# Kernel optimization log

Measured on AMD Instinct MI355X. Metric: run time of the kernel, lower is better.

The kernel has to match this reference:

```python
import jax, jax.numpy as jnp
import numpy as np
from jax import lax

_CLIP_MIN = 1e-06
_CLIP_MAX = 1.0
_POS_ALPHA = 0.0005
NUM_CLASSES = 21
RADIUS = 3
HALF_D = RADIUS * RADIUS
POOL = 3
PAD = POOL // 2
IGNORE = 255
LAM = 0.5  # loss_weight_lambda, lambda_way=1


def _max_pool(x):
    # NCHW max pool, kernel=stride=3, padding=1
    return lax.reduce_window(x, -jnp.inf, lax.max,
                             (1, 1, POOL, POOL), (1, 1, POOL, POOL),
                             ((0, 0), (0, 0), (PAD, PAD), (PAD, PAD)))


def _get_pairs(x):
    # stack radius*radius shifted crops -> [N, C, r^2, nh, nw]
    h, w = x.shape[2], x.shape[3]
    nh, nw = h - RADIUS + 1, w - RADIUS + 1
    crops = [x[:, :, y:y + nh, xo:xo + nw] for y in range(RADIUS) for xo in range(RADIUS)]
    return jnp.stack(crops, axis=2)


def _log_det_by_cholesky(m):
    chol = jnp.linalg.cholesky(m)
    return 2.0 * jnp.sum(jnp.log(jnp.diagonal(chol, axis1=-2, axis2=-1) + 1e-08), axis=-1)


def _rmi_lower_bound(labels_4d, probs_4d):
    la = _max_pool(labels_4d)
    pr = _max_pool(probs_4d)
    n, c = la.shape[0], la.shape[1]
    la_v = _get_pairs(la).reshape(n, c, HALF_D, -1)   # [N,C,d,L]
    pr_v = _get_pairs(pr).reshape(n, c, HALF_D, -1)
    la_v = la_v - jnp.mean(la_v, axis=3, keepdims=True)
    pr_v = pr_v - jnp.mean(pr_v, axis=3, keepdims=True)
    la_cov = jnp.einsum('ncdl,ncel->ncde', la_v, la_v)
    pr_cov = jnp.einsum('ncdl,ncel->ncde', pr_v, pr_v)
    eye = jnp.eye(HALF_D, dtype=la_cov.dtype)
    pr_cov_inv = jnp.linalg.inv(pr_cov + eye * _POS_ALPHA)
    la_pr_cov = jnp.einsum('ncdl,ncel->ncde', la_v, pr_v)
    appro_var = la_cov - jnp.einsum('ncde,ncef,ncgf->ncdg', la_pr_cov, pr_cov_inv, la_pr_cov)
    rmi_now = 0.5 * _log_det_by_cholesky(appro_var + eye * _POS_ALPHA)  # [N,C]
    rmi_per_class = jnp.mean(rmi_now.reshape(-1, NUM_CLASSES), axis=0) / float(HALF_D)
    return jnp.sum(rmi_per_class)


def setup_inputs() -> dict:
    key = jax.random.key(0)
    k1, k2 = jax.random.split(key)
    score = jax.random.normal(k1, (4, NUM_CLASSES, 512, 512), dtype=jnp.float32)
    target = jax.random.randint(k2, (4, 512, 512), 0, NUM_CLASSES, dtype=jnp.int64)
    return {"score": score, "target": target}


def reference(score, target):
    # cross entropy with ignore_index=255, mean reduction
    logp = jax.nn.log_softmax(score, axis=1)                      # [N,C,H,W]
    valid_ce = (target != IGNORE)
    safe_t = jnp.where(valid_ce, target, 0)
    nll = -jnp.take_along_axis(logp, safe_t[:, None].astype(jnp.int32), axis=1)[:, 0]
    normal_loss = jnp.sum(jnp.where(valid_ce, nll, 0.0)) / jnp.sum(valid_ce.astype(jnp.float32))

    # valid one-hot labels and masked sigmoid probs
    mask = (target < NUM_CLASSES)                                 # [N,H,W]
    maskf = mask.astype(jnp.float32)
    onehot = jax.nn.one_hot((target * mask).astype(jnp.int32), NUM_CLASSES, dtype=jnp.float32)
    onehot = onehot * maskf[..., None]                            # [N,H,W,C]
    onehot = jnp.transpose(onehot, (0, 3, 1, 2))                  # [N,C,H,W]
    probs = jnp.clip(jax.nn.sigmoid(score) * maskf[:, None], _CLIP_MIN, _CLIP_MAX)

    rmi_loss = _rmi_lower_bound(onehot, probs)
    return LAM * normal_loss + rmi_loss * (1.0 - LAM)
```

## Files before the change

kernel.cpp:

```cpp
#include <hip/hip_runtime.h>
#include <cfloat>
#include <cmath>

#define DEVINL __device__ __forceinline__

constexpr int N_ = 4, C_ = 21, H_ = 512, W_ = 512;
constexpr int P_ = 171;
constexpr int Q_ = 169;
constexpr int NC_ = N_ * C_;
constexpr int HW_ = H_ * W_;
constexpr int PP_ = 29241;
constexpr int PROW_ = 192;
constexpr int PPAD_ = PROW_ * P_;
constexpr int NCOV_ = 189;
constexpr float EPS_ = 5e-4f;
constexpr int RC_ = 43;
constexpr int G_ = 43;
constexpr int HMROW_ = 172;
constexpr int HMPL_ = 512 * HMROW_;

constexpr int NB_CE = 1024;
constexpr int NB_PL = (NC_ * P_ * G_ + 255) / 256;

typedef float f4_t __attribute__((ext_vector_type(4)));
typedef __attribute__((address_space(1))) const void gas_void;
typedef __attribute__((address_space(3))) void las_void;

DEVINL constexpr int tstart(int d) { return d * 9 - d * (d - 1) / 2; }

template <int CTRL>
DEVINL float dpp_add(float v) {
    int x = __builtin_amdgcn_update_dpp(0, __float_as_int(v), CTRL, 0xF, 0xF, false);
    return v + __int_as_float(x);
}

DEVINL float wave_sum63(float v) {
    v = dpp_add<0x111>(v);
    v = dpp_add<0x112>(v);
    v = dpp_add<0x114>(v);
    v = dpp_add<0x118>(v);
    v = dpp_add<0x142>(v);
    v = dpp_add<0x143>(v);
    return v;
}

__global__ __launch_bounds__(256) void k_bits(const int* __restrict__ target,
                                              unsigned* __restrict__ pack,
                                              float* __restrict__ cov) {
    int t = threadIdx.x;
    if (blockIdx.x == 0) {
        for (int k = t; k < NC_ * NCOV_ + 2; k += 256) cov[k] = 0.f;
    }
    int tid = blockIdx.x * 256 + t;
    if (tid >= N_ * PP_) return;
    int cell = tid % PP_;
    int n = tid / PP_;
    int j = cell % P_;
    int i = cell / P_;
    int hl = 3 * i - 1; if (hl < 0) hl = 0;
    int wl = 3 * j - 1; if (wl < 0) wl = 0;
    int hmax = 3 * i + 1, wmax = 3 * j + 1;
    const int* tb = target + (size_t)n * HW_;
    unsigned oh = 0, px = 0;
#pragma unroll
    for (int r = 0; r < 3; ++r) {
        int hh = hl + r;
        bool hv = hh <= hmax;
        const int* trow = tb + hh * W_;
#pragma unroll
        for (int dc = 0; dc < 3; ++dc) {
            int ww = wl + dc;
            int tv = trow[ww];
            if (hv && (ww <= wmax) && tv >= 0 && tv < C_) {
                oh |= 1u << tv;
                px |= 1u << (r * 3 + dc);
            }
        }
    }
    pack[tid] = oh | (px << 23);
}

__global__ __launch_bounds__(256) void k_ce2(const float* __restrict__ score,
                                             const int* __restrict__ target,
                                             float* __restrict__ hm,
                                             float* __restrict__ cov) {
    __shared__ float lds[4 * 1024];
    __shared__ unsigned char lval[1024];
    __shared__ float rn[4], rc[4];
    int b = blockIdx.x;
    int t = threadIdx.x;
    int wv = t >> 6, lane = t & 63;
    int n = b >> 8;
    int brow = (b & 255) * 2;
    int bhw = brow * W_;
    const float* sp0 = score + (size_t)n * C_ * HW_ + bhw;

    int4 t4 = *(const int4*)(target + (size_t)n * HW_ + bhw + t * 4);
    unsigned vb = (unsigned)(t4.x >= 0 && t4.x < C_)
                | ((unsigned)(t4.y >= 0 && t4.y < C_) << 8)
                | ((unsigned)(t4.z >= 0 && t4.z < C_) << 16)
                | ((unsigned)(t4.w >= 0 && t4.w < C_) << 24);
    *(unsigned*)&lval[t * 4] = vb;

    float4 se = {0.f, 0.f, 0.f, 0.f};
    float4 stgt = {0.f, 0.f, 0.f, 0.f};
    float* hmn = hm + (size_t)n * C_ * HMPL_ + (size_t)brow * HMROW_;

    for (int ph = 0; ph < 6; ++ph) {
        int c0 = ph * 4;
        int np = (c0 + 4 <= C_) ? 4 : (C_ - c0);
        if (wv < np) {
            int c = c0 + wv;
#pragma unroll
            for (int k = 0; k < 4; ++k) {
                const float* g = sp0 + (size_t)c * HW_ + k * 256 + lane * 4;
                float* l = &lds[wv * 1024 + k * 256];
                __builtin_amdgcn_global_load_lds((gas_void*)g, (las_void*)l,
                                                 16, 0, 0);
            }
        }
        asm volatile("s_waitcnt vmcnt(0)" ::: "memory");
        __syncthreads();

        for (int u = 0; u < np; ++u) {
            int cc = c0 + u;
            f4_t v = *(const f4_t*)&lds[u * 1024 + t * 4];
            se.x += __expf(v.x);
            se.y += __expf(v.y);
            se.z += __expf(v.z);
            se.w += __expf(v.w);
            if (t4.x == cc) stgt.x = v.x;
            if (t4.y == cc) stgt.y = v.y;
            if (t4.z == cc) stgt.z = v.z;
            if (t4.w == cc) stgt.w = v.w;
        }

        int nit = np * 342;
        for (int it = t; it < nit; it += 256) {
            int u = it / 342;
            int rem = it - u * 342;
            int r = rem / 171;
            int j = rem - r * 171;
            int wl = 3 * j - 1; if (wl < 0) wl = 0;
            int wmax = 3 * j + 1;
            const float* ls = &lds[u * 1024 + r * 512];
            const unsigned char* lv = &lval[r * 512];
            float m = -FLT_MAX;
#pragma unroll
            for (int dc = 0; dc < 3; ++dc) {
                int ww = wl + dc;
                if (ww <= wmax && lv[ww]) m = fmaxf(m, ls[ww]);
            }
            hmn[(size_t)(c0 + u) * HMPL_ + (size_t)r * HMROW_ + j] = m;
        }
        __syncthreads();
    }

    float nll = 0.f, cnt = 0.f;
    if (t4.x != 255) { nll += __logf(se.x) - stgt.x; cnt += 1.f; }
    if (t4.y != 255) { nll += __logf(se.y) - stgt.y; cnt += 1.f; }
    if (t4.z != 255) { nll += __logf(se.z) - stgt.z; cnt += 1.f; }
    if (t4.w != 255) { nll += __logf(se.w) - stgt.w; cnt += 1.f; }

    nll = wave_sum63(nll);
    cnt = wave_sum63(cnt);
    if (lane == 63) { rn[wv] = nll; rc[wv] = cnt; }
    __syncthreads();
    if (t == 0)
        atomicAdd(&cov[NC_ * NCOV_ + 0], rn[0] + rn[1] + rn[2] + rn[3]);
    if (t == 64)
        atomicAdd(&cov[NC_ * NCOV_ + 1], rc[0] + rc[1] + rc[2] + rc[3]);
}

__global__ __launch_bounds__(256) void k_pool2(const float* __restrict__ hm,
                                               const unsigned* __restrict__ pack,
                                               float* __restrict__ pr,
                                               float* __restrict__ la) {
    int tid = blockIdx.x * 256 + threadIdx.x;
    if (tid >= NC_ * P_ * G_) return;
    int g = tid % G_;
    int rest = tid / G_;
    int i = rest % P_;
    int ncidx = rest / P_;
    int n = ncidx / C_;
    int c = ncidx - n * C_;

    int hl = 3 * i - 1; if (hl < 0) hl = 0;
    int nr = (i == 0) ? 2 : 3;
    const float* hp = hm + (size_t)ncidx * HMPL_ + (size_t)hl * HMROW_ + 4 * g;
    f4_t m = {-FLT_MAX, -FLT_MAX, -FLT_MAX, -FLT_MAX};
    for (int rr = 0; rr < nr; ++rr) {
        f4_t v = *(const f4_t*)(hp + (size_t)rr * HMROW_);
        m.x = fmaxf(m.x, v.x);
        m.y = fmaxf(m.y, v.y);
        m.z = fmaxf(m.z, v.z);
        m.w = fmaxf(m.w, v.w);
    }
    const unsigned* pkp = pack + n * PP_ + i * P_ + 4 * g;
    size_t ob = (size_t)ncidx * PPAD_ + (size_t)i * PROW_ + 4 * g;

    float p0 = fminf(fmaxf(__builtin_amdgcn_rcpf(1.f + __expf(-m.x)), 1e-6f), 1.f);
    float p1 = fminf(fmaxf(__builtin_amdgcn_rcpf(1.f + __expf(-m.y)), 1e-6f), 1.f);
    float p2 = fminf(fmaxf(__builtin_amdgcn_rcpf(1.f + __expf(-m.z)), 1e-6f), 1.f);
    pr[ob + 0] = p0; la[ob + 0] = ((pkp[0] >> c) & 1u) ? 1.f : 0.f;
    pr[ob + 1] = p1; la[ob + 1] = ((pkp[1] >> c) & 1u) ? 1.f : 0.f;
    pr[ob + 2] = p2; la[ob + 2] = ((pkp[2] >> c) & 1u) ? 1.f : 0.f;
    if (4 * g + 3 < P_) {
        float p3 = fminf(fmaxf(__builtin_amdgcn_rcpf(1.f + __expf(-m.w)), 1e-6f), 1.f);
        pr[ob + 3] = p3; la[ob + 3] = ((pkp[3] >> c) & 1u) ? 1.f : 0.f;
    }
}

template <int D0, int D1>
DEVINL void cov_tri(const float* __restrict__ X, float* __restrict__ cov,
                    int nc, int r0, int rend, int s2base,
                    int tid, float (*red)[27]) {
    constexpr int NS2 = ((9 - D0) * (10 - D0) - (9 - D1) * (10 - D1)) / 2;
    constexpr int RLO = D0 / 3;
    constexpr int KOFF = tstart(D0);
    float s2[NS2];
#pragma unroll
    for (int k = 0; k < NS2; ++k) s2[k] = 0.f;

    int nitems = (rend - r0) * G_;
    for (int idx = tid; idx < nitems; idx += 256) {
        int lr = idx / G_;
        int q = idx - lr * G_;
        int x0 = q * 4;
        const float* base = X + (size_t)(r0 + lr) * PROW_ + x0;
        float v[3][8];
#pragma unroll
        for (int r = RLO; r < 3; ++r) {
            float4 u0 = *(const float4*)(base + r * PROW_);
            float4 u1 = *(const float4*)(base + r * PROW_ + 4);
            v[r][0] = u0.x; v[r][1] = u0.y; v[r][2] = u0.z; v[r][3] = u0.w;
            v[r][4] = u1.x; v[r][5] = u1.y; v[r][6] = u1.z; v[r][7] = u1.w;
        }
#pragma unroll
        for (int p = 0; p < 4; ++p) {
            if (x0 + p < Q_) {
                int k = 0;
#pragma unroll
                for (int d = D0; d < D1; ++d)
#pragma unroll
                    for (int e = d; e < 9; ++e) {
                        s2[k] += v[d / 3][p + d % 3] * v[e / 3][p + e % 3];
                        ++k;
                    }
            }
        }
    }

    int lane = tid & 63, wv = tid >> 6;
#pragma unroll
    for (int k = 0; k < NS2; ++k) {
        float v2 = wave_sum63(s2[k]);
        if (lane == 63) red[wv][k] = v2;
    }
    __syncthreads();
    if (tid < NS2) {
        float v2 = red[0][tid] + red[1][tid] + red[2][tid] + red[3][tid];
        atomicAdd(&cov[nc * NCOV_ + s2base + KOFF + tid], v2);
    }
}

template <int RA>
DEVINL void cov_ab(const float* __restrict__ A, const float* __restrict__ B,
                   float* __restrict__ cov, int nc, int r0, int rend,
                   int tid, float (*red)[27]) {
    float sab[27];
#pragma unroll
    for (int k = 0; k < 27; ++k) sab[k] = 0.f;

    int nitems = (rend - r0) * G_;
    for (int idx = tid; idx < nitems; idx += 256) {
        int lr = idx / G_;
        int q = idx - lr * G_;
        int x0 = q * 4;
        size_t off = (size_t)(r0 + lr) * PROW_ + x0;
        float a[8];
        {
            float4 u0 = *(const float4*)(A + off + RA * PROW_);
            float4 u1 = *(const float4*)(A + off + RA * PROW_ + 4);
            a[0] = u0.x; a[1] = u0.y; a[2] = u0.z; a[3] = u0.w;
            a[4] = u1.x; a[5] = u1.y; a[6] = u1.z; a[7] = u1.w;
        }
#pragma unroll
        for (int r = 0; r < 3; ++r) {
            float b[8];
            {
                float4 w0 = *(const float4*)(B + off + r * PROW_);
                float4 w1 = *(const float4*)(B + off + r * PROW_ + 4);
                b[0] = w0.x; b[1] = w0.y; b[2] = w0.z; b[3] = w0.w;
                b[4] = w1.x; b[5] = w1.y; b[6] = w1.z; b[7] = w1.w;
            }
#pragma unroll
            for (int p = 0; p < 4; ++p) {
                if (x0 + p < Q_) {
#pragma unroll
                    for (int dm = 0; dm < 3; ++dm)
#pragma unroll
                        for (int e2 = 0; e2 < 3; ++e2)
                            sab[dm * 9 + r * 3 + e2] += a[p + dm] * b[p + e2];
                }
            }
        }
    }

    int lane = tid & 63, wv = tid >> 6;
#pragma unroll
    for (int k = 0; k < 27; ++k) {
        float v2 = wave_sum63(sab[k]);
        if (lane == 63) red[wv][k] = v2;
    }
    __syncthreads();
    if (tid < 27) {
        float v2 = red[0][tid] + red[1][tid] + red[2][tid] + red[3][tid];
        atomicAdd(&cov[nc * NCOV_ + 108 + RA * 27 + tid], v2);
    }
}

DEVINL void cov_s1(const float* __restrict__ LA, const float* __restrict__ PR,
                   float* __restrict__ cov, int nc, int r0, int rend,
                   int tid, float (*red)[27]) {
    float s1a[9], s1b[9];
#pragma unroll
    for (int k = 0; k < 9; ++k) { s1a[k] = 0.f; s1b[k] = 0.f; }

    int nitems = (rend - r0) * G_;
    for (int idx = tid; idx < nitems; idx += 256) {
        int lr = idx / G_;
        int q = idx - lr * G_;
        int x0 = q * 4;
        size_t off = (size_t)(r0 + lr) * PROW_ + x0;
#pragma unroll
        for (int r = 0; r < 3; ++r) {
            float va[8], vb[8];
            {
                float4 u0 = *(const float4*)(LA + off + r * PROW_);
                float4 u1 = *(const float4*)(LA + off + r * PROW_ + 4);
                va[0] = u0.x; va[1] = u0.y; va[2] = u0.z; va[3] = u0.w;
                va[4] = u1.x; va[5] = u1.y; va[6] = u1.z; va[7] = u1.w;
                float4 w0 = *(const float4*)(PR + off + r * PROW_);
                float4 w1 = *(const float4*)(PR + off + r * PROW_ + 4);
                vb[0] = w0.x; vb[1] = w0.y; vb[2] = w0.z; vb[3] = w0.w;
                vb[4] = w1.x; vb[5] = w1.y; vb[6] = w1.z; vb[7] = w1.w;
            }
#pragma unroll
            for (int p = 0; p < 4; ++p) {
                if (x0 + p < Q_) {
#pragma unroll
                    for (int dc = 0; dc < 3; ++dc) {
                        s1a[r * 3 + dc] += va[p + dc];
                        s1b[r * 3 + dc] += vb[p + dc];
                    }
                }
            }
        }
    }

    int lane = tid & 63, wv = tid >> 6;
#pragma unroll
    for (int k = 0; k < 9; ++k) {
        float v2 = wave_sum63(s1a[k]);
        if (lane == 63) red[wv][k] = v2;
    }
#pragma unroll
    for (int k = 0; k < 9; ++k) {
        float v2 = wave_sum63(s1b[k]);
        if (lane == 63) red[wv][9 + k] = v2;
    }
    __syncthreads();
    if (tid < 18) {
        float v2 = red[0][tid] + red[1][tid] + red[2][tid] + red[3][tid];
        atomicAdd(&cov[nc * NCOV_ + tid], v2);
    }
}

__global__ __launch_bounds__(256) void k_cov(const float* __restrict__ la,
                                             const float* __restrict__ pr,
                                             float* __restrict__ cov) {
    __shared__ float red[4][27];
    int nc = blockIdx.x;
    int chunk = blockIdx.y;
    int part = blockIdx.z;
    int r0 = chunk * RC_;
    int rend = r0 + RC_;
    if (rend > Q_) rend = Q_;
    int tid = threadIdx.x;
    const float* LA = la + (size_t)nc * PPAD_;
    const float* PR = pr + (size_t)nc * PPAD_;

    switch (part) {
        case 0: cov_tri<0, 3>(LA, cov, nc, r0, rend, 18, tid, red); break;
        case 1: cov_tri<3, 9>(LA, cov, nc, r0, rend, 18, tid, red); break;
        case 2: cov_tri<0, 3>(PR, cov, nc, r0, rend, 63, tid, red); break;
        case 3: cov_tri<3, 9>(PR, cov, nc, r0, rend, 63, tid, red); break;
        case 4: cov_ab<0>(LA, PR, cov, nc, r0, rend, tid, red); break;
        case 5: cov_ab<1>(LA, PR, cov, nc, r0, rend, tid, red); break;
        case 6: cov_ab<2>(LA, PR, cov, nc, r0, rend, tid, red); break;
        case 7: cov_s1(LA, PR, cov, nc, r0, rend, tid, red); break;
    }
}

__global__ __launch_bounds__(128) void k_final(const float* __restrict__ cov,
                                               float* __restrict__ out) {
    __shared__ float red[128];
    int t = threadIdx.x;
    float my = 0.f;
    if (t < NC_) {
        const float* S = cov + t * NCOV_;
        const float Lf = (float)(Q_ * Q_);
        float sA[9], sB[9];
#pragma unroll
        for (int d = 0; d < 9; ++d) { sA[d] = S[d]; sB[d] = S[9 + d]; }
        float laC[45], M[45], Cm[81];
        {
            int k = 0;
#pragma unroll
            for (int d = 0; d < 9; ++d)
#pragma unroll
                for (int e = d; e < 9; ++e) {
                    laC[k] = S[18 + k] - sA[d] * sA[e] / Lf;
                    M[k] = S[63 + k] - sB[d] * sB[e] / Lf + (d == e ? EPS_ : 0.f);
                    ++k;
                }
#pragma unroll
            for (int d = 0; d < 9; ++d)
#pragma unroll
                for (int e = 0; e < 9; ++e)
                    Cm[d * 9 + e] = S[108 + d * 9 + e] - sA[d] * sB[e] / Lf;
        }
#pragma unroll
        for (int j = 0; j < 9; ++j) {
            float s = M[tstart(j)];
#pragma unroll
            for (int k = 0; k < j; ++k) { float l = M[tstart(k) + (j - k)]; s -= l * l; }
            float dj = sqrtf(fmaxf(s, 1e-30f));
            M[tstart(j)] = dj;
            float inv = 1.f / dj;
#pragma unroll
            for (int i = j + 1; i < 9; ++i) {
                float s2 = M[tstart(j) + (i - j)];
#pragma unroll
                for (int k = 0; k < j; ++k)
                    s2 -= M[tstart(k) + (i - k)] * M[tstart(k) + (j - k)];
                M[tstart(j) + (i - j)] = s2 * inv;
            }
        }
#pragma unroll
        for (int p = 0; p < 9; ++p) {
#pragma unroll
            for (int i = 0; i < 9; ++i) {
                float s = Cm[p * 9 + i];
#pragma unroll
                for (int k = 0; k < i; ++k)
                    s -= M[tstart(k) + (i - k)] * Cm[p * 9 + k];
                Cm[p * 9 + i] = s / M[tstart(i)];
            }
        }
#pragma unroll
        for (int d = 0; d < 9; ++d)
#pragma unroll
            for (int e = d; e < 9; ++e) {
                float s = 0.f;
#pragma unroll
                for (int i = 0; i < 9; ++i) s += Cm[d * 9 + i] * Cm[e * 9 + i];
                laC[tstart(d) + (e - d)] -= s;
                if (d == e) laC[tstart(d)] += EPS_;
            }
        float rmi = 0.f;
#pragma unroll
        for (int j = 0; j < 9; ++j) {
            float s = laC[tstart(j)];
#pragma unroll
            for (int k = 0; k < j; ++k) { float l = laC[tstart(k) + (j - k)]; s -= l * l; }
            float dj = sqrtf(fmaxf(s, 0.f));
            laC[tstart(j)] = dj;
            float inv = 1.f / fmaxf(dj, 1e-30f);
#pragma unroll
            for (int i = j + 1; i < 9; ++i) {
                float s2 = laC[tstart(j) + (i - j)];
#pragma unroll
                for (int k = 0; k < j; ++k)
                    s2 -= laC[tstart(k) + (i - k)] * laC[tstart(k) + (j - k)];
                laC[tstart(j) + (i - j)] = s2 * inv;
            }
            rmi += __logf(dj + 1e-8f);
        }
        my = rmi;
    }
    red[t] = my;
    __syncthreads();
#pragma unroll
    for (int o = 64; o > 0; o >>= 1) {
        if (t < o) red[t] += red[t + o];
        __syncthreads();
    }
    if (t == 0) {
        float rmi_total = red[0] / 36.f;
        float ce = cov[NC_ * NCOV_ + 0] / cov[NC_ * NCOV_ + 1];
        out[0] = 0.5f * ce + 0.5f * rmi_total;
    }
}

extern "C" void kernel_launch(void* const* d_in, const int* in_sizes, int n_in,
                              void* d_out, int out_size, void* d_ws, size_t ws_size,
                              hipStream_t stream) {
    const float* score = (const float*)d_in[0];
    const int* target = (const int*)d_in[1];
    float* pr = (float*)d_ws;
    float* la = pr + (size_t)NC_ * PPAD_;
    float* hm = la + (size_t)NC_ * PPAD_;
    float* cov = hm + (size_t)NC_ * HMPL_;
    unsigned* pack = (unsigned*)(cov + NC_ * NCOV_ + 2);

    k_bits<<<dim3((N_ * PP_ + 255) / 256), dim3(256), 0, stream>>>(target, pack, cov);
    k_ce2<<<dim3(NB_CE), dim3(256), 0, stream>>>(score, target, hm, cov);
    k_pool2<<<dim3(NB_PL), dim3(256), 0, stream>>>(hm, pack, pr, la);
    k_cov<<<dim3(NC_, 4, 8), dim3(256), 0, stream>>>(la, pr, cov);
    k_final<<<dim3(1), dim3(128), 0, stream>>>(cov, (float*)d_out);
}
```

Measured before the change: 251.4 us.

## Restructure covariance kernel into row-strip sliding window with fused moment accumulation

Replaces the eight-way split of the covariance kernel, where each block recomputed a subset of moments by reloading three rows per item, with three parts (label triangle plus sums, prob triangle plus sums, cross block). Each thread now walks a vertical strip of rows, keeping a rolling window of four rows in registers so every row is loaded once and reused across three window positions. This cuts global loads and removes the separate first-moment pass, at the cost of much larger per-thread accumulators (54 or 81 registers), fewer blocks (192 threads, 3 parts), and idle threads beyond 172.

```diff
diff --git a/kernel.cpp b/kernel.cpp
--- a/kernel.cpp
+++ b/kernel.cpp
@@ -14,7 +14,6 @@
 constexpr int PPAD_ = PROW_ * P_;
 constexpr int NCOV_ = 189;
 constexpr float EPS_ = 5e-4f;
-constexpr int RC_ = 43;
 constexpr int G_ = 43;
 constexpr int HMROW_ = 172;
 constexpr int HMPL_ = 512 * HMROW_;
@@ -211,195 +210,172 @@
     }
 }
 
-template <int D0, int D1>
-DEVINL void cov_tri(const float* __restrict__ X, float* __restrict__ cov,
-                    int nc, int r0, int rend, int s2base,
-                    int tid, float (*red)[27]) {
-    constexpr int NS2 = ((9 - D0) * (10 - D0) - (9 - D1) * (10 - D1)) / 2;
-    constexpr int RLO = D0 / 3;
-    constexpr int KOFF = tstart(D0);
-    float s2[NS2];
-#pragma unroll
-    for (int k = 0; k < NS2; ++k) s2[k] = 0.f;
-
-    int nitems = (rend - r0) * G_;
-    for (int idx = tid; idx < nitems; idx += 256) {
-        int lr = idx / G_;
-        int q = idx - lr * G_;
-        int x0 = q * 4;
-        const float* base = X + (size_t)(r0 + lr) * PROW_ + x0;
-        float v[3][8];
-#pragma unroll
-        for (int r = RLO; r < 3; ++r) {
-            float4 u0 = *(const float4*)(base + r * PROW_);
-            float4 u1 = *(const float4*)(base + r * PROW_ + 4);
-            v[r][0] = u0.x; v[r][1] = u0.y; v[r][2] = u0.z; v[r][3] = u0.w;
-            v[r][4] = u1.x; v[r][5] = u1.y; v[r][6] = u1.z; v[r][7] = u1.w;
-        }
-#pragma unroll
-        for (int p = 0; p < 4; ++p) {
-            if (x0 + p < Q_) {
-                int k = 0;
-#pragma unroll
-                for (int d = D0; d < D1; ++d)
-#pragma unroll
-                    for (int e = d; e < 9; ++e) {
-                        s2[k] += v[d / 3][p + d % 3] * v[e / 3][p + e % 3];
-                        ++k;
-                    }
-            }
+DEVINL void ldrow(float (&dst)[8], const float* Xb, int row) {
+    const float* p = Xb + (size_t)row * PROW_;
+    f4_t u0 = *(const f4_t*)p;
+    f4_t u1 = *(const f4_t*)(p + 4);
+    dst[0] = u0.x; dst[1] = u0.y; dst[2] = u0.z; dst[3] = u0.w;
+    dst[4] = u1.x; dst[5] = u1.y; dst[6] = u1.z; dst[7] = u1.w;
+}
+
+DEVINL void tri_step(float (&acc)[54], const float (&A)[8], const float (&B)[8],
+                     const float (&C)[8], int x0) {
+#pragma unroll
+    for (int p = 0; p < 4; ++p) {
+        if (x0 + p < Q_) {
+            float v[9] = {A[p], A[p + 1], A[p + 2], B[p], B[p + 1], B[p + 2],
+                          C[p], C[p + 1], C[p + 2]};
+#pragma unroll
+            for (int d = 0; d < 9; ++d) acc[d] += v[d];
+            int k = 9;
+#pragma unroll
+            for (int d = 0; d < 9; ++d)
+#pragma unroll
+                for (int e = d; e < 9; ++e) { acc[k] += v[d] * v[e]; ++k; }
+        }
+    }
+}
+
+DEVINL void ab_step(float (&acc)[81], const float (&A0)[8], const float (&A1)[8],
+                    const float (&A2)[8], const float (&B0)[8], const float (&B1)[8],
+                    const float (&B2)[8], int x0) {
+#pragma unroll
+    for (int p = 0; p < 4; ++p) {
+        if (x0 + p < Q_) {
+            float v[9] = {A0[p], A0[p + 1], A0[p + 2], A1[p], A1[p + 1], A1[p + 2],
+                          A2[p], A2[p + 1], A2[p + 2]};
+            float w[9] = {B0[p], B0[p + 1], B0[p + 2], B1[p], B1[p + 1], B1[p + 2],
+                          B2[p], B2[p + 1], B2[p + 2]};
+#pragma unroll
+            for (int d = 0; d < 9; ++d)
+#pragma unroll
+                for (int e = 0; e < 9; ++e) acc[d * 9 + e] += v[d] * w[e];
+        }
+    }
+}
+
+DEVINL void cov_tri_strip(const float* __restrict__ X, float* __restrict__ cov,
+                          int nc, int r0, int rend, int s1base, int s2base,
+                          int tid, float (*red)[81]) {
+    float acc[54];
+#pragma unroll
+    for (int k = 0; k < 54; ++k) acc[k] = 0.f;
+
+    if (tid < 4 * G_) {
+        int s = tid / G_, q = tid - s * G_;
+        int len = rend - r0, sl = (len + 3) >> 2;
+        int a0 = r0 + s * sl;
+        int a1 = a0 + sl; if (a1 > rend) a1 = rend;
+        if (a0 < a1) {
+            int x0 = 4 * q;
+            const float* Xb = X + x0;
+            float R0[8], R1[8], R2[8], R3[8];
+            ldrow(R0, Xb, a0); ldrow(R1, Xb, a0 + 1); ldrow(R2, Xb, a0 + 2);
+            int i = a0;
+            while (i + 4 <= a1) {
+                ldrow(R3, Xb, i + 3);                       tri_step(acc, R0, R1, R2, x0);
+                ldrow(R0, Xb, i + 4);                       tri_step(acc, R1, R2, R3, x0);
+                ldrow(R1, Xb, i + 5);                       tri_step(acc, R2, R3, R0, x0);
+                ldrow(R2, Xb, (i + 6 < P_) ? i + 6 : P_ - 1); tri_step(acc, R3, R0, R1, x0);
+                i += 4;
+            }
+            int rem = a1 - i;
+            if (rem >= 1) tri_step(acc, R0, R1, R2, x0);
+            if (rem >= 2) { ldrow(R3, Xb, i + 3); tri_step(acc, R1, R2, R3, x0); }
+            if (rem >= 3) { ldrow(R0, Xb, (i + 4 < P_) ? i + 4 : P_ - 1);
+                            tri_step(acc, R2, R3, R0, x0); }
         }
     }
 
     int lane = tid & 63, wv = tid >> 6;
 #pragma unroll
-    for (int k = 0; k < NS2; ++k) {
-        float v2 = wave_sum63(s2[k]);
+    for (int k = 0; k < 54; ++k) {
+        float v2 = wave_sum63(acc[k]);
         if (lane == 63) red[wv][k] = v2;
     }
     __syncthreads();
-    if (tid < NS2) {
-        float v2 = red[0][tid] + red[1][tid] + red[2][tid] + red[3][tid];
-        atomicAdd(&cov[nc * NCOV_ + s2base + KOFF + tid], v2);
-    }
-}
-
-template <int RA>
-DEVINL void cov_ab(const float* __restrict__ A, const float* __restrict__ B,
-                   float* __restrict__ cov, int nc, int r0, int rend,
-                   int tid, float (*red)[27]) {
-    float sab[27];
-#pragma unroll
-    for (int k = 0; k < 27; ++k) sab[k] = 0.f;
-
-    int nitems = (rend - r0) * G_;
-    for (int idx = tid; idx < nitems; idx += 256) {
-        int lr = idx / G_;
-        int q = idx - lr * G_;
-        int x0 = q * 4;
-        size_t off = (size_t)(r0 + lr) * PROW_ + x0;
-        float a[8];
-        {
-            float4 u0 = *(const float4*)(A + off + RA * PROW_);
-            float4 u1 = *(const float4*)(A + off + RA * PROW_ + 4);
-            a[0] = u0.x; a[1] = u0.y; a[2] = u0.z; a[3] = u0.w;
-            a[4] = u1.x; a[5] = u1.y; a[6] = u1.z; a[7] = u1.w;
-        }
-#pragma unroll
-        for (int r = 0; r < 3; ++r) {
-            float b[8];
-            {
-                float4 w0 = *(const float4*)(B + off + r * PROW_);
-                float4 w1 = *(const float4*)(B + off + r * PROW_ + 4);
-                b[0] = w0.x; b[1] = w0.y; b[2] = w0.z; b[3] = w0.w;
-                b[4] = w1.x; b[5] = w1.y; b[6] = w1.z; b[7] = w1.w;
-            }
-#pragma unroll
-            for (int p = 0; p < 4; ++p) {
-                if (x0 + p < Q_) {
-#pragma unroll
-                    for (int dm = 0; dm < 3; ++dm)
-#pragma unroll
-                        for (int e2 = 0; e2 < 3; ++e2)
-                            sab[dm * 9 + r * 3 + e2] += a[p + dm] * b[p + e2];
-                }
-            }
+    if (tid < 54) {
+        float v2 = red[0][tid] + red[1][tid] + red[2][tid];
+        int dst = (tid < 9) ? (s1base + tid) : (s2base + tid - 9);
+        atomicAdd(&cov[nc * NCOV_ + dst], v2);
+    }
+}
+
+DEVINL void cov_ab_strip(const float* __restrict__ LA, const float* __restrict__ PR,
+                         float* __restrict__ cov, int nc, int r0, int rend,
+                         int tid, float (*red)[81]) {
+    float acc[81];
+#pragma unroll
+    for (int k = 0; k < 81; ++k) acc[k] = 0.f;
+
+    if (tid < 4 * G_) {
+        int s = tid / G_, q = tid - s * G_;
+        int len = rend - r0, sl = (len + 3) >> 2;
+        int a0 = r0 + s * sl;
+        int a1 = a0 + sl; if (a1 > rend) a1 = rend;
+        if (a0 < a1) {
+            int x0 = 4 * q;
+            const float* Lb = LA + x0;
+            const float* Pb = PR + x0;
+            float L0[8], L1[8], L2[8], L3[8];
+            float Pv0[8], Pv1[8], Pv2[8], Pv3[8];
+            ldrow(L0, Lb, a0);     ldrow(Pv0, Pb, a0);
+            ldrow(L1, Lb, a0 + 1); ldrow(Pv1, Pb, a0 + 1);
+            ldrow(L2, Lb, a0 + 2); ldrow(Pv2, Pb, a0 + 2);
+            int i = a0;
+            while (i + 4 <= a1) {
+                ldrow(L3, Lb, i + 3); ldrow(Pv3, Pb, i + 3);
+                ab_step(acc, L0, L1, L2, Pv0, Pv1, Pv2, x0);
+                ldrow(L0, Lb, i + 4); ldrow(Pv0, Pb, i + 4);
+                ab_step(acc, L1, L2, L3, Pv1, Pv2, Pv3, x0);
+                ldrow(L1, Lb, i + 5); ldrow(Pv1, Pb, i + 5);
+                ab_step(acc, L2, L3, L0, Pv2, Pv3, Pv0, x0);
+                int pre = (i + 6 < P_) ? i + 6 : P_ - 1;
+                ldrow(L2, Lb, pre); ldrow(Pv2, Pb, pre);
+                ab_step(acc, L3, L0, L1, Pv3, Pv0, Pv1, x0);
+                i += 4;
+            }
+            int rem = a1 - i;
+            if (rem >= 1) ab_step(acc, L0, L1, L2, Pv0, Pv1, Pv2, x0);
+            if (rem >= 2) { ldrow(L3, Lb, i + 3); ldrow(Pv3, Pb, i + 3);
+                            ab_step(acc, L1, L2, L3, Pv1, Pv2, Pv3, x0); }
+            if (rem >= 3) { int pre = (i + 4 < P_) ? i + 4 : P_ - 1;
+                            ldrow(L0, Lb, pre); ldrow(Pv0, Pb, pre);
+                            ab_step(acc, L2, L3, L0, Pv2, Pv3, Pv0, x0); }
         }
     }
 
     int lane = tid & 63, wv = tid >> 6;
 #pragma unroll
-    for (int k = 0; k < 27; ++k) {
-        float v2 = wave_sum63(sab[k]);
+    for (int k = 0; k < 81; ++k) {
+        float v2 = wave_sum63(acc[k]);
         if (lane == 63) red[wv][k] = v2;
     }
     __syncthreads();
-    if (tid < 27) {
-        float v2 = red[0][tid] + red[1][tid] + red[2][tid] + red[3][tid];
-        atomicAdd(&cov[nc * NCOV_ + 108 + RA * 27 + tid], v2);
-    }
-}
-
-DEVINL void cov_s1(const float* __restrict__ LA, const float* __restrict__ PR,
-                   float* __restrict__ cov, int nc, int r0, int rend,
-                   int tid, float (*red)[27]) {
-    float s1a[9], s1b[9];
-#pragma unroll
-    for (int k = 0; k < 9; ++k) { s1a[k] = 0.f; s1b[k] = 0.f; }
-
-    int nitems = (rend - r0) * G_;
-    for (int idx = tid; idx < nitems; idx += 256) {
-        int lr = idx / G_;
-        int q = idx - lr * G_;
-        int x0 = q * 4;
-        size_t off = (size_t)(r0 + lr) * PROW_ + x0;
-#pragma unroll
-        for (int r = 0; r < 3; ++r) {
-            float va[8], vb[8];
-            {
-                float4 u0 = *(const float4*)(LA + off + r * PROW_);
-                float4 u1 = *(const float4*)(LA + off + r * PROW_ + 4);
-                va[0] = u0.x; va[1] = u0.y; va[2] = u0.z; va[3] = u0.w;
-                va[4] = u1.x; va[5] = u1.y; va[6] = u1.z; va[7] = u1.w;
-                float4 w0 = *(const float4*)(PR + off + r * PROW_);
-                float4 w1 = *(const float4*)(PR + off + r * PROW_ + 4);
-                vb[0] = w0.x; vb[1] = w0.y; vb[2] = w0.z; vb[3] = w0.w;
-                vb[4] = w1.x; vb[5] = w1.y; vb[6] = w1.z; vb[7] = w1.w;
-            }
-#pragma unroll
-            for (int p = 0; p < 4; ++p) {
-                if (x0 + p < Q_) {
-#pragma unroll
-                    for (int dc = 0; dc < 3; ++dc) {
-                        s1a[r * 3 + dc] += va[p + dc];
-                        s1b[r * 3 + dc] += vb[p + dc];
-                    }
-                }
-            }
-        }
-    }
-
-    int lane = tid & 63, wv = tid >> 6;
-#pragma unroll
-    for (int k = 0; k < 9; ++k) {
-        float v2 = wave_sum63(s1a[k]);
-        if (lane == 63) red[wv][k] = v2;
-    }
-#pragma unroll
-    for (int k = 0; k < 9; ++k) {
-        float v2 = wave_sum63(s1b[k]);
-        if (lane == 63) red[wv][9 + k] = v2;
-    }
-    __syncthreads();
-    if (tid < 18) {
-        float v2 = red[0][tid] + red[1][tid] + red[2][tid] + red[3][tid];
-        atomicAdd(&cov[nc * NCOV_ + tid], v2);
-    }
-}
-
-__global__ __launch_bounds__(256) void k_cov(const float* __restrict__ la,
-                                             const float* __restrict__ pr,
-                                             float* __restrict__ cov) {
-    __shared__ float red[4][27];
+    if (tid < 81) {
+        float v2 = red[0][tid] + red[1][tid] + red[2][tid];
+        atomicAdd(&cov[nc * NCOV_ + 108 + tid], v2);
+    }
+}
+
+__global__ __launch_bounds__(192, 2) void k_cov(const float* __restrict__ la,
+                                                const float* __restrict__ pr,
+                                                float* __restrict__ cov) {
+    __shared__ float red[3][81];
     int nc = blockIdx.x;
     int chunk = blockIdx.y;
     int part = blockIdx.z;
-    int r0 = chunk * RC_;
-    int rend = r0 + RC_;
+    int r0 = chunk * 43;
+    int rend = r0 + 43;
     if (rend > Q_) rend = Q_;
     int tid = threadIdx.x;
     const float* LA = la + (size_t)nc * PPAD_;
     const float* PR = pr + (size_t)nc * PPAD_;
 
     switch (part) {
-        case 0: cov_tri<0, 3>(LA, cov, nc, r0, rend, 18, tid, red); break;
-        case 1: cov_tri<3, 9>(LA, cov, nc, r0, rend, 18, tid, red); break;
-        case 2: cov_tri<0, 3>(PR, cov, nc, r0, rend, 63, tid, red); break;
-        case 3: cov_tri<3, 9>(PR, cov, nc, r0, rend, 63, tid, red); break;
-        case 4: cov_ab<0>(LA, PR, cov, nc, r0, rend, tid, red); break;
-        case 5: cov_ab<1>(LA, PR, cov, nc, r0, rend, tid, red); break;
-        case 6: cov_ab<2>(LA, PR, cov, nc, r0, rend, tid, red); break;
-        case 7: cov_s1(LA, PR, cov, nc, r0, rend, tid, red); break;
+        case 0: cov_tri_strip(LA, cov, nc, r0, rend, 0, 18, tid, red); break;
+        case 1: cov_tri_strip(PR, cov, nc, r0, rend, 9, 63, tid, red); break;
+        case 2: cov_ab_strip(LA, PR, cov, nc, r0, rend, tid, red); break;
     }
 }
 
@@ -518,6 +494,6 @@
     k_bits<<<dim3((N_ * PP_ + 255) / 256), dim3(256), 0, stream>>>(target, pack, cov);
     k_ce2<<<dim3(NB_CE), dim3(256), 0, stream>>>(score, target, hm, cov);
     k_pool2<<<dim3(NB_PL), dim3(256), 0, stream>>>(hm, pack, pr, la);
-    k_cov<<<dim3(NC_, 4, 8), dim3(256), 0, stream>>>(la, pr, cov);
+    k_cov<<<dim3(NC_, 4, 3), dim3(192), 0, stream>>>(la, pr, cov);
     k_final<<<dim3(1), dim3(128), 0, stream>>>(cov, (float*)d_out);
 }
```

Result: faster. 234.6 us (-6.7%).
